# Performance work log

Measured on AMD Instinct MI355X. Metric: run time of the kernel, lower is better.

The kernel has to match this reference:

```python
import jax, jax.numpy as jnp
import numpy as np

B, N, C = 4, 4000, 91          # images, proposals/image, classes (incl. background)
H = W = 800                    # image shape
WX, WY, WW, WH = 10.0, 10.0, 5.0, 5.0   # bbox_reg_weights
BBOX_CLIP = float(np.log(1000.0 / 16.0))
SCORE_T = 0.05
NMS_T = 0.5
DETS = 100                     # detections_per_img
MIN_SIZE = 0.01
NEG = jnp.float32(-1e30)
M = N * (C - 1)                # candidates per image after dropping background


def setup_inputs() -> dict:
    key = jax.random.key(0)
    k1, k2, k3, k4 = jax.random.split(key, 4)
    class_logits = jax.random.normal(k1, (B * N, C), jnp.float32)
    box_regression = jax.random.normal(k2, (B * N, C * 4), jnp.float32)
    # valid proposals: x1<x2, y1<y2, inside the image
    ctr = jax.random.uniform(k3, (B, N, 2), jnp.float32, 0.0, 800.0)
    wh = jax.random.uniform(k4, (B, N, 2), jnp.float32, 16.0, 256.0)
    x1y1 = jnp.clip(ctr - 0.5 * wh, 0.0, 800.0)
    x2y2 = jnp.clip(ctr + 0.5 * wh, 0.0, 800.0)
    proposals = jnp.concatenate([x1y1, x2y2], axis=-1)
    return {"class_logits": class_logits, "box_regression": box_regression,
            "proposals": proposals}


def _decode(rel, props):
    # rel: [B,N,C,4] deltas, props: [B,N,4] -> per-class boxes [B,N,C,4]
    widths = props[..., 2] - props[..., 0]
    heights = props[..., 3] - props[..., 1]
    ctr_x = props[..., 0] + 0.5 * widths
    ctr_y = props[..., 1] + 0.5 * heights
    dx = rel[..., 0] / WX
    dy = rel[..., 1] / WY
    dw = jnp.minimum(rel[..., 2] / WW, BBOX_CLIP)
    dh = jnp.minimum(rel[..., 3] / WH, BBOX_CLIP)
    pcx = dx * widths[..., None] + ctr_x[..., None]
    pcy = dy * heights[..., None] + ctr_y[..., None]
    pw = jnp.exp(dw) * widths[..., None]
    ph = jnp.exp(dh) * heights[..., None]
    return jnp.stack([pcx - 0.5 * pw, pcy - 0.5 * ph,
                      pcx + 0.5 * pw, pcy + 0.5 * ph], axis=-1)


def _iou_one(box, boxes):
    # box [4] vs boxes [M,4]
    lt = jnp.maximum(box[:2], boxes[:, :2])
    rb = jnp.minimum(box[2:], boxes[:, 2:])
    wh = jnp.clip(rb - lt, 0.0)
    inter = wh[:, 0] * wh[:, 1]
    a1 = (box[2] - box[0]) * (box[3] - box[1])
    a2 = (boxes[:, 2] - boxes[:, 0]) * (boxes[:, 3] - boxes[:, 1])
    return inter / (a1 + a2 - inter)


def _nms_image(boxes_off, scores_m):
    # greedy NMS on class-offset boxes; returns DETS indices + validity flags
    idxs = jnp.arange(scores_m.shape[0])

    def step(scores_rem, _):
        best = jnp.argmax(scores_rem)
        bscore = scores_rem[best]
        iou = _iou_one(boxes_off[best], boxes_off)
        sup = (iou > NMS_T) | (idxs == best)
        return jnp.where(sup, NEG, scores_rem), (best, bscore > NEG * 0.5)

    _, (keep_idx, keep_ok) = jax.lax.scan(step, scores_m, None, length=DETS)
    return keep_idx, keep_ok


def reference(class_logits, box_regression, proposals):
    logits = class_logits.reshape(B, N, C)
    rel = box_regression.reshape(B, N, C, 4)
    boxes = _decode(rel, proposals)                       # [B,N,C,4]
    # clip_boxes_to_image
    boxes = jnp.stack([jnp.clip(boxes[..., 0], 0.0, W),
                       jnp.clip(boxes[..., 1], 0.0, H),
                       jnp.clip(boxes[..., 2], 0.0, W),
                       jnp.clip(boxes[..., 3], 0.0, H)], axis=-1)
    scores = jax.nn.softmax(logits, axis=-1)              # [B,N,C]
    # drop background class 0, flatten per-image candidates
    cand_boxes = boxes[:, :, 1:, :].reshape(B, M, 4)
    cand_scores = scores[:, :, 1:].reshape(B, M)
    labels = jnp.tile(jnp.arange(1, C, dtype=jnp.int32), N)   # [M]
    # score threshold + remove_small_boxes
    ws = cand_boxes[..., 2] - cand_boxes[..., 0]
    hs = cand_boxes[..., 3] - cand_boxes[..., 1]
    valid = (cand_scores > SCORE_T) & (ws >= MIN_SIZE) & (hs >= MIN_SIZE)
    scores_m = jnp.where(valid, cand_scores, NEG)
    # batched_nms: offset boxes per class so cross-class boxes never overlap
    offs = labels.astype(jnp.float32) * (W + 1.0)
    boxes_off = cand_boxes + offs[None, :, None]
    keep_idx, keep_ok = jax.vmap(_nms_image)(boxes_off, scores_m)  # [B,DETS]
    out_boxes = jnp.take_along_axis(cand_boxes, keep_idx[..., None], axis=1)
    out_scores = jnp.take_along_axis(cand_scores, keep_idx, axis=1)
    out_labels = labels[keep_idx]
    out_boxes = jnp.where(keep_ok[..., None], out_boxes, 0.0)
    out_scores = jnp.where(keep_ok, out_scores, 0.0)
    out_labels = jnp.where(keep_ok, out_labels, 0)
    return out_boxes, out_scores, out_labels, keep_ok
```

## Files before the change

kernel.cpp:

```cpp
#include <hip/hip_runtime.h>

#define Bc 4
#define Nc 4000
#define Cc 91
#define SEGW 20
#define BCAP 64
#define SELTGT 512
#define DETS 100
#define NBIN 4096
#define SELCAP 1024

typedef unsigned long long u64;

__device__ __forceinline__ float4 decode_box(const float4 r, float w, float h,
                                             float cx, float cy) {
    const float BBOX_CLIP = 4.135166556742356f;
    float dx = r.x / 10.f, dy = r.y / 10.f;
    float dw = fminf(r.z / 5.f, BBOX_CLIP);
    float dh = fminf(r.w / 5.f, BBOX_CLIP);
    float pcx = dx * w + cx, pcy = dy * h + cy;
    float pw = expf(dw) * w, ph = expf(dh) * h;
    float4 o;
    o.x = fminf(fmaxf(pcx - 0.5f * pw, 0.f), 800.f);
    o.y = fminf(fmaxf(pcy - 0.5f * ph, 0.f), 800.f);
    o.z = fminf(fmaxf(pcx + 0.5f * pw, 0.f), 800.f);
    o.w = fminf(fmaxf(pcy + 0.5f * ph, 0.f), 800.f);
    return o;
}

__global__ __launch_bounds__(256) void compact_k(
    const float* __restrict__ logits, const float* __restrict__ regs,
    const float* __restrict__ props, ulonglong2* __restrict__ pmask,
    unsigned* __restrict__ scoreseg, int* __restrict__ ghist,
    int* __restrict__ bcnt, int* __restrict__ done) {
    if (blockIdx.x < 16) {
        int base = blockIdx.x * 1024;
#pragma unroll
        for (int j = 0; j < 4; ++j)
            ghist[base + j * 256 + threadIdx.x] = 0;
    } else if (blockIdx.x == 16) {
        int t = threadIdx.x;
        bcnt[t] = 0;
        if (t < Bc * Cc - 256) bcnt[256 + t] = 0;
        if (t == 0) *done = 0;
    }
    const int wv = threadIdx.x >> 6;
    const int ln = threadIdx.x & 63;
    const int pA = blockIdx.x * 8 + wv * 2;
    const int pB = pA + 1;

    const float* lA = logits + (size_t)pA * Cc;
    const float* lB = logits + (size_t)pB * Cc;
    float a0 = lA[ln];
    float b0 = lB[ln];
    float a1 = (ln < Cc - 64) ? lA[64 + ln] : -1e30f;
    float b1 = (ln < Cc - 64) ? lB[64 + ln] : -1e30f;
    const float4 prA = *reinterpret_cast<const float4*>(props + 4 * (size_t)pA);
    const float4 prB = *reinterpret_cast<const float4*>(props + 4 * (size_t)pB);

    float mA = fmaxf(a0, a1), mB = fmaxf(b0, b1);
#pragma unroll
    for (int off = 32; off; off >>= 1) {
        mA = fmaxf(mA, __shfl_xor(mA, off));
        mB = fmaxf(mB, __shfl_xor(mB, off));
    }
    float eA0 = expf(a0 - mA), eB0 = expf(b0 - mB);
    float eA1 = (ln < Cc - 64) ? expf(a1 - mA) : 0.f;
    float eB1 = (ln < Cc - 64) ? expf(b1 - mB) : 0.f;
    float sA = eA0 + eA1, sB = eB0 + eB1;
#pragma unroll
    for (int off = 32; off; off >>= 1) {
        sA += __shfl_xor(sA, off);
        sB += __shfl_xor(sB, off);
    }

    const float wA = prA.z - prA.x, hA = prA.w - prA.y;
    const float cxA = prA.x + 0.5f * wA, cyA = prA.y + 0.5f * hA;
    const float wB = prB.z - prB.x, hB = prB.w - prB.y;
    const float cxB = prB.x + 0.5f * wB, cyB = prB.y + 0.5f * hB;

    float vA0 = eA0 / sA, vB0 = eB0 / sB, vA1 = eA1 / sA, vB1 = eB1 / sB;
    bool fA0 = false, fA1 = false, fB0 = false, fB1 = false;
    if (ln >= 1 && vA0 > 0.05f) {
        float4 r = *reinterpret_cast<const float4*>(
            regs + ((size_t)pA * Cc + ln) * 4);
        float4 bx = decode_box(r, wA, hA, cxA, cyA);
        fA0 = (bx.z - bx.x >= 0.01f) && (bx.w - bx.y >= 0.01f);
    }
    if (ln >= 1 && vB0 > 0.05f) {
        float4 r = *reinterpret_cast<const float4*>(
            regs + ((size_t)pB * Cc + ln) * 4);
        float4 bx = decode_box(r, wB, hB, cxB, cyB);
        fB0 = (bx.z - bx.x >= 0.01f) && (bx.w - bx.y >= 0.01f);
    }
    if (ln < Cc - 64 && vA1 > 0.05f) {
        float4 r = *reinterpret_cast<const float4*>(
            regs + ((size_t)pA * Cc + 64 + ln) * 4);
        float4 bx = decode_box(r, wA, hA, cxA, cyA);
        fA1 = (bx.z - bx.x >= 0.01f) && (bx.w - bx.y >= 0.01f);
    }
    if (ln < Cc - 64 && vB1 > 0.05f) {
        float4 r = *reinterpret_cast<const float4*>(
            regs + ((size_t)pB * Cc + 64 + ln) * 4);
        float4 bx = decode_box(r, wB, hB, cxB, cyB);
        fB1 = (bx.z - bx.x >= 0.01f) && (bx.w - bx.y >= 0.01f);
    }

    const u64 below = (1ULL << ln) - 1ULL;
    u64 mA0 = __ballot(fA0), mA1 = __ballot(fA1);
    u64 mB0 = __ballot(fB0), mB1 = __ballot(fB1);
    int cA0 = __popcll(mA0), cB0 = __popcll(mB0);
    if (fA0) scoreseg[(size_t)pA * SEGW + __popcll(mA0 & below)] =
        __float_as_uint(vA0);
    if (fA1) scoreseg[(size_t)pA * SEGW + cA0 + __popcll(mA1 & below)] =
        __float_as_uint(vA1);
    if (fB0) scoreseg[(size_t)pB * SEGW + __popcll(mB0 & below)] =
        __float_as_uint(vB0);
    if (fB1) scoreseg[(size_t)pB * SEGW + cB0 + __popcll(mB1 & below)] =
        __float_as_uint(vB1);
    if (ln == 0) {
        pmask[pA] = make_ulonglong2(mA0, mA1);
        pmask[pB] = make_ulonglong2(mB0, mB1);
    }
}

__global__ __launch_bounds__(256) void histsel_k(
    const ulonglong2* __restrict__ pmask, const unsigned* __restrict__ scoreseg,
    int* __restrict__ ghist, int* __restrict__ done,
    u64* __restrict__ bucket, int* __restrict__ bcnt) {
    __shared__ int hist[NBIN];
    __shared__ int thrS;
    const int b = blockIdx.x >> 4;
    const int sub = blockIdx.x & 15;
    const int t = threadIdx.x;

    for (int i = t; i < NBIN; i += 256) hist[i] = 0;
    __syncthreads();
    if (t < 250) {
        int p = b * Nc + sub * 250 + t;
        ulonglong2 pm = pmask[p];
        int nk = __popcll(pm.x) + __popcll(pm.y);
        for (int j = 0; j < nk; ++j)
            atomicAdd(&hist[scoreseg[(size_t)p * SEGW + j] >> 20], 1);
    }
    __syncthreads();
    for (int i = t; i < NBIN; i += 256) {
        int v = hist[i];
        if (v) atomicAdd(&ghist[b * NBIN + i], v);
    }
    __syncthreads();

    if (t == 0) {
        __threadfence();
        atomicAdd(done, 1);
        while (atomicAdd(done, 0) < 64) __builtin_amdgcn_s_sleep(8);
        __threadfence();
    }
    __syncthreads();

    if (t < 64) {
        const int ln = t;
        const int* h = ghist + b * NBIN;
        int loc[64];
        int tot = 0;
#pragma unroll
        for (int j = 0; j < 64; ++j) { loc[j] = h[ln * 64 + j]; tot += loc[j]; }
        int inc = tot;
#pragma unroll
        for (int off = 1; off < 64; off <<= 1) {
            int v = __shfl_down(inc, off);
            if (ln + off < 64) inc += v;
        }
        int cum = inc - tot;
        int myThr = -1;
#pragma unroll
        for (int j = 63; j >= 0; --j) {
            if (cum < SELTGT && cum + loc[j] >= SELTGT) myThr = ln * 64 + j;
            cum += loc[j];
        }
#pragma unroll
        for (int off = 32; off; off >>= 1)
            myThr = max(myThr, __shfl_xor(myThr, off));
        if (ln == 0) thrS = (myThr < 0) ? 0 : myThr;
    }
    __syncthreads();
    const int th = thrS;

    if (t < 250) {
        int p = b * Nc + sub * 250 + t;
        const ulonglong2 pm = pmask[p];
        if (pm.x | pm.y) {
            const int n = p - b * Nc;
            int idx = 0;
#pragma unroll
            for (int rnd = 0; rnd < 2; ++rnd) {
                u64 mm = rnd ? pm.y : pm.x;
                while (mm) {
                    int j = __ffsll((long long)mm) - 1; mm &= mm - 1;
                    int c = j + rnd * 64;
                    unsigned sb = scoreseg[(size_t)p * SEGW + idx]; ++idx;
                    if ((int)(sb >> 20) >= th) {
                        unsigned m = (unsigned)(n * 90 + (c - 1));
                        u64 key = ((u64)sb << 32) |
                                  ((u64)(1048575u - m) << 12) | (u64)c;
                        int sl = atomicAdd(&bcnt[b * Cc + c], 1);
                        if (sl < BCAP) bucket[(b * Cc + c) * BCAP + sl] = key;
                    }
                }
            }
        }
    }
}

__global__ __launch_bounds__(64) void nmsc_k(
    u64* __restrict__ bucket, const int* __restrict__ bcnt,
    const float* __restrict__ regs, const float* __restrict__ props,
    int* __restrict__ kkc) {
    const int b = blockIdx.x / (Cc - 1);
    const int c = 1 + blockIdx.x % (Cc - 1);
    const int ln = threadIdx.x;
    const int nc = min(bcnt[b * Cc + c], BCAP);
    bool alive = ln < nc;
    u64 lk = alive ? bucket[(b * Cc + c) * BCAP + ln] : 0ULL;
    float4 bx = make_float4(0.f, 0.f, 0.f, 0.f);
    float area = 0.f;
    if (alive) {
        int m = 1048575 - (int)((lk >> 12) & 0xFFFFFULL);
        int n = m / (Cc - 1);
        int p = b * Nc + n;
        const float4 pr = *reinterpret_cast<const float4*>(props + 4 * (size_t)p);
        float w = pr.z - pr.x, h = pr.w - pr.y;
        float cx = pr.x + 0.5f * w, cy = pr.y + 0.5f * h;
        const float4 r = *reinterpret_cast<const float4*>(
            regs + ((size_t)p * Cc + c) * 4);
        bx = decode_box(r, w, h, cx, cy);
        float off_ = (float)c * 801.0f;
        bx.x += off_; bx.y += off_; bx.z += off_; bx.w += off_;
        area = (bx.z - bx.x) * (bx.w - bx.y);
    }

    int nk = 0;
    for (;;) {
        u64 m = alive ? lk : 0ULL;
#pragma unroll
        for (int off = 32; off; off >>= 1) {
            u64 o = __shfl_xor(m, off);
            m = (o > m) ? o : m;
        }
        if (m == 0ULL) break;
        u64 wmask = __ballot(alive && lk == m);
        int wl = __ffsll((long long)wmask) - 1;
        if (ln == wl) bucket[(b * Cc + c) * BCAP + nk] = m;
        ++nk;
        float wx1 = __shfl(bx.x, wl), wy1 = __shfl(bx.y, wl);
        float wx2 = __shfl(bx.z, wl), wy2 = __shfl(bx.w, wl);
        float wa = __shfl(area, wl);
        if (alive) {
            if (lk == m) {
                alive = false;
            } else {
                float iw = fmaxf(fminf(wx2, bx.z) - fmaxf(wx1, bx.x), 0.f);
                float ih = fmaxf(fminf(wy2, bx.w) - fmaxf(wy1, bx.y), 0.f);
                float inter = iw * ih;
                float iou = inter / (wa + area - inter);
                if (iou > 0.5f) alive = false;
            }
        }
    }
    if (ln == 0) kkc[b * Cc + c] = nk;
}

__global__ __launch_bounds__(1024) void top100_k(
    const u64* __restrict__ bucket, const int* __restrict__ kkc,
    const float* __restrict__ regs, const float* __restrict__ props,
    float* __restrict__ out) {
    __shared__ u64 sKey[SELCAP];
    __shared__ u64 sTop[DETS];
    __shared__ int cnts[Cc], offs[Cc + 1];
    const int b = blockIdx.x, t = threadIdx.x;
    const int ln = t & 63, wv = t >> 6;

    if (t < Cc)
        cnts[t] = (t == 0) ? 0 : min(max(kkc[b * Cc + t], 0), BCAP);
    if (t < DETS) sTop[t] = 0ULL;
    __syncthreads();
    if (t == 0) {
        int acc = 0;
        for (int c = 0; c < Cc; ++c) { offs[c] = acc; acc += cnts[c]; }
        offs[Cc] = acc;
    }
    __syncthreads();
    const int total = min(offs[Cc], SELCAP);

    for (int c = wv; c < Cc; c += 16) {
        int k = cnts[c];
        if (ln < k) {
            int d = offs[c] + ln;
            if (d >= 0 && d < SELCAP)
                sKey[d] = bucket[(b * Cc + c) * BCAP + ln];
        }
    }
    __syncthreads();

    for (int i = t; i < total; i += 1024) {
        u64 k = sKey[i];
        int r = 0;
#pragma unroll 4
        for (int j = 0; j < total; ++j) r += (sKey[j] > k) ? 1 : 0;
        if (r < DETS) sTop[r] = k;
    }
    __syncthreads();

    if (t < DETS) {
        int o = b * DETS + t;
        u64 k = sTop[t];
        float* ob = out + (size_t)o * 4;
        if (k != 0ULL) {
            int lab = (int)(k & 0xFFFULL);
            int m = 1048575 - (int)((k >> 12) & 0xFFFFFULL);
            int n = m / (Cc - 1);
            int c = m - n * (Cc - 1) + 1;
            int p = b * Nc + n;
            const float4 pr =
                *reinterpret_cast<const float4*>(props + 4 * (size_t)p);
            const float w = pr.z - pr.x, h = pr.w - pr.y;
            const float cx = pr.x + 0.5f * w, cy = pr.y + 0.5f * h;
            const float4 r4 = *reinterpret_cast<const float4*>(
                regs + ((size_t)p * Cc + c) * 4);
            float4 bx = decode_box(r4, w, h, cx, cy);
            ob[0] = bx.x; ob[1] = bx.y; ob[2] = bx.z; ob[3] = bx.w;
            out[Bc * DETS * 4 + o] = __uint_as_float((unsigned)(k >> 32));
            out[Bc * DETS * 5 + o] = (float)lab;
            out[Bc * DETS * 6 + o] = 1.0f;
        } else {
            ob[0] = ob[1] = ob[2] = ob[3] = 0.f;
            out[Bc * DETS * 4 + o] = 0.f;
            out[Bc * DETS * 5 + o] = 0.f;
            out[Bc * DETS * 6 + o] = 0.f;
        }
    }
}

extern "C" void kernel_launch(void* const* d_in, const int* in_sizes, int n_in,
                              void* d_out, int out_size, void* d_ws, size_t ws_size,
                              hipStream_t stream) {
    const float* logits = (const float*)d_in[0];
    const float* regs   = (const float*)d_in[1];
    const float* props  = (const float*)d_in[2];
    float* out = (float*)d_out;

    char* ws = (char*)d_ws;
    size_t o = 0;
    ulonglong2* pmask = (ulonglong2*)(ws + o); o += (size_t)Bc * Nc * 16;
    unsigned* scoreseg = (unsigned*)(ws + o);  o += (size_t)Bc * Nc * SEGW * 4;
    u64* bucket  = (u64*)(ws + o);             o += (size_t)Bc * Cc * BCAP * 8;
    int* ghist   = (int*)(ws + o);             o += (size_t)Bc * NBIN * 4;
    int* bcnt    = (int*)(ws + o);             o += (size_t)Bc * Cc * 4;
    int* kkc     = (int*)(ws + o);             o += (size_t)Bc * Cc * 4;
    int* done    = (int*)(ws + o);

    hipLaunchKernelGGL(compact_k, dim3(Bc * Nc / 8), dim3(256), 0, stream,
                       logits, regs, props, pmask, scoreseg, ghist, bcnt, done);
    hipLaunchKernelGGL(histsel_k, dim3(Bc * 16), dim3(256), 0, stream,
                       pmask, scoreseg, ghist, done, bucket, bcnt);
    hipLaunchKernelGGL(nmsc_k, dim3(Bc * (Cc - 1)), dim3(64), 0, stream,
                       bucket, bcnt, regs, props, kkc);
    hipLaunchKernelGGL(top100_k, dim3(Bc), dim3(1024), 0, stream,
                       bucket, kkc, regs, props, out);
}
```

Baseline: 55.26 us.

## Fuse histogram-select, per-class NMS and top-100 into one persistent kernel

Merges the histogram/threshold-select kernel, the per-class NMS kernel and the final top-100 kernel into a single 64-block kernel that uses atomic-counter grid barriers between phases. Each wave runs NMS for one or two classes, and one block per image does the final rank selection with 256 threads instead of 1024. The aim is to remove two kernel launches and their gaps. In exchange, NMS gets fewer concurrent waves, the top-100 rank sort has less parallelism, and the spin barriers assume all 64 blocks are co-resident.

```diff
diff --git a/kernel.cpp b/kernel.cpp
--- a/kernel.cpp
+++ b/kernel.cpp
@@ -9,6 +9,7 @@
 #define DETS 100
 #define NBIN 4096
 #define SELCAP 1024
+#define MEGABLK 64
 
 typedef unsigned long long u64;
 
@@ -42,7 +43,7 @@
         int t = threadIdx.x;
         bcnt[t] = 0;
         if (t < Bc * Cc - 256) bcnt[256 + t] = 0;
-        if (t == 0) *done = 0;
+        if (t < 3) done[t] = 0;
     }
     const int wv = threadIdx.x >> 6;
     const int ln = threadIdx.x & 63;
@@ -124,64 +125,70 @@
     }
 }
 
-__global__ __launch_bounds__(256) void histsel_k(
+__device__ __forceinline__ void grid_sync(int* ctr) {
+    __syncthreads();
+    if (threadIdx.x == 0) {
+        __threadfence();
+        atomicAdd(ctr, 1);
+        while (atomicAdd(ctr, 0) < MEGABLK) __builtin_amdgcn_s_sleep(2);
+        __threadfence();
+    }
+    __syncthreads();
+}
+
+__global__ __launch_bounds__(256) void mega_k(
     const ulonglong2* __restrict__ pmask, const unsigned* __restrict__ scoreseg,
-    int* __restrict__ ghist, int* __restrict__ done,
-    u64* __restrict__ bucket, int* __restrict__ bcnt) {
-    __shared__ int hist[NBIN];
+    int* __restrict__ ghist, int* __restrict__ done, u64* __restrict__ bucket,
+    int* __restrict__ bcnt, int* __restrict__ kkc,
+    const float* __restrict__ regs, const float* __restrict__ props,
+    float* __restrict__ out) {
+    __shared__ __align__(16) int shm[NBIN];
     __shared__ int thrS;
     const int b = blockIdx.x >> 4;
     const int sub = blockIdx.x & 15;
     const int t = threadIdx.x;
-
-    for (int i = t; i < NBIN; i += 256) hist[i] = 0;
+    const int ln = t & 63, wv = t >> 6;
+
+    for (int i = t; i < NBIN; i += 256) shm[i] = 0;
     __syncthreads();
     if (t < 250) {
         int p = b * Nc + sub * 250 + t;
         ulonglong2 pm = pmask[p];
         int nk = __popcll(pm.x) + __popcll(pm.y);
         for (int j = 0; j < nk; ++j)
-            atomicAdd(&hist[scoreseg[(size_t)p * SEGW + j] >> 20], 1);
+            atomicAdd(&shm[scoreseg[(size_t)p * SEGW + j] >> 20], 1);
     }
     __syncthreads();
     for (int i = t; i < NBIN; i += 256) {
-        int v = hist[i];
+        int v = shm[i];
         if (v) atomicAdd(&ghist[b * NBIN + i], v);
     }
-    __syncthreads();
-
-    if (t == 0) {
-        __threadfence();
-        atomicAdd(done, 1);
-        while (atomicAdd(done, 0) < 64) __builtin_amdgcn_s_sleep(8);
-        __threadfence();
-    }
-    __syncthreads();
+    grid_sync(&done[0]);
 
     if (t < 64) {
-        const int ln = t;
+        const int l = t;
         const int* h = ghist + b * NBIN;
         int loc[64];
         int tot = 0;
 #pragma unroll
-        for (int j = 0; j < 64; ++j) { loc[j] = h[ln * 64 + j]; tot += loc[j]; }
+        for (int j = 0; j < 64; ++j) { loc[j] = h[l * 64 + j]; tot += loc[j]; }
         int inc = tot;
 #pragma unroll
         for (int off = 1; off < 64; off <<= 1) {
             int v = __shfl_down(inc, off);
-            if (ln + off < 64) inc += v;
+            if (l + off < 64) inc += v;
         }
         int cum = inc - tot;
         int myThr = -1;
 #pragma unroll
         for (int j = 63; j >= 0; --j) {
-            if (cum < SELTGT && cum + loc[j] >= SELTGT) myThr = ln * 64 + j;
+            if (cum < SELTGT && cum + loc[j] >= SELTGT) myThr = l * 64 + j;
             cum += loc[j];
         }
 #pragma unroll
         for (int off = 32; off; off >>= 1)
             myThr = max(myThr, __shfl_xor(myThr, off));
-        if (ln == 0) thrS = (myThr < 0) ? 0 : myThr;
+        if (l == 0) thrS = (myThr < 0) ? 0 : myThr;
     }
     __syncthreads();
     const int th = thrS;
@@ -210,78 +217,78 @@
             }
         }
     }
-}
-
-__global__ __launch_bounds__(64) void nmsc_k(
-    u64* __restrict__ bucket, const int* __restrict__ bcnt,
-    const float* __restrict__ regs, const float* __restrict__ props,
-    int* __restrict__ kkc) {
-    const int b = blockIdx.x / (Cc - 1);
-    const int c = 1 + blockIdx.x % (Cc - 1);
-    const int ln = threadIdx.x;
-    const int nc = min(bcnt[b * Cc + c], BCAP);
-    bool alive = ln < nc;
-    u64 lk = alive ? bucket[(b * Cc + c) * BCAP + ln] : 0ULL;
-    float4 bx = make_float4(0.f, 0.f, 0.f, 0.f);
-    float area = 0.f;
-    if (alive) {
-        int m = 1048575 - (int)((lk >> 12) & 0xFFFFFULL);
-        int n = m / (Cc - 1);
-        int p = b * Nc + n;
-        const float4 pr = *reinterpret_cast<const float4*>(props + 4 * (size_t)p);
-        float w = pr.z - pr.x, h = pr.w - pr.y;
-        float cx = pr.x + 0.5f * w, cy = pr.y + 0.5f * h;
-        const float4 r = *reinterpret_cast<const float4*>(
-            regs + ((size_t)p * Cc + c) * 4);
-        bx = decode_box(r, w, h, cx, cy);
-        float off_ = (float)c * 801.0f;
-        bx.x += off_; bx.y += off_; bx.z += off_; bx.w += off_;
-        area = (bx.z - bx.x) * (bx.w - bx.y);
-    }
-
-    int nk = 0;
-    for (;;) {
-        u64 m = alive ? lk : 0ULL;
-#pragma unroll
-        for (int off = 32; off; off >>= 1) {
-            u64 o = __shfl_xor(m, off);
-            m = (o > m) ? o : m;
-        }
-        if (m == 0ULL) break;
-        u64 wmask = __ballot(alive && lk == m);
-        int wl = __ffsll((long long)wmask) - 1;
-        if (ln == wl) bucket[(b * Cc + c) * BCAP + nk] = m;
-        ++nk;
-        float wx1 = __shfl(bx.x, wl), wy1 = __shfl(bx.y, wl);
-        float wx2 = __shfl(bx.z, wl), wy2 = __shfl(bx.w, wl);
-        float wa = __shfl(area, wl);
+    grid_sync(&done[1]);
+
+    const int wid = sub * 4 + wv;
+#pragma unroll
+    for (int rep = 0; rep < 2; ++rep) {
+        if (rep == 1 && wid >= 26) break;
+        const int c = (rep == 0) ? (1 + wid) : (65 + wid);
+        const int nc = min(bcnt[b * Cc + c], BCAP);
+        bool alive = ln < nc;
+        u64 lk = alive ? bucket[(b * Cc + c) * BCAP + ln] : 0ULL;
+        float4 bx = make_float4(0.f, 0.f, 0.f, 0.f);
+        float area = 0.f;
         if (alive) {
-            if (lk == m) {
-                alive = false;
-            } else {
-                float iw = fmaxf(fminf(wx2, bx.z) - fmaxf(wx1, bx.x), 0.f);
-                float ih = fmaxf(fminf(wy2, bx.w) - fmaxf(wy1, bx.y), 0.f);
-                float inter = iw * ih;
-                float iou = inter / (wa + area - inter);
-                if (iou > 0.5f) alive = false;
+            int m = 1048575 - (int)((lk >> 12) & 0xFFFFFULL);
+            int n = m / (Cc - 1);
+            int p = b * Nc + n;
+            const float4 pr =
+                *reinterpret_cast<const float4*>(props + 4 * (size_t)p);
+            float w = pr.z - pr.x, h = pr.w - pr.y;
+            float cx = pr.x + 0.5f * w, cy = pr.y + 0.5f * h;
+            const float4 r = *reinterpret_cast<const float4*>(
+                regs + ((size_t)p * Cc + c) * 4);
+            bx = decode_box(r, w, h, cx, cy);
+            float off_ = (float)c * 801.0f;
+            bx.x += off_; bx.y += off_; bx.z += off_; bx.w += off_;
+            area = (bx.z - bx.x) * (bx.w - bx.y);
+        }
+        int nk = 0;
+        for (;;) {
+            u64 m = alive ? lk : 0ULL;
+#pragma unroll
+            for (int off = 32; off; off >>= 1) {
+                u64 o = __shfl_xor(m, off);
+                m = (o > m) ? o : m;
             }
-        }
-    }
-    if (ln == 0) kkc[b * Cc + c] = nk;
-}
-
-__global__ __launch_bounds__(1024) void top100_k(
-    const u64* __restrict__ bucket, const int* __restrict__ kkc,
-    const float* __restrict__ regs, const float* __restrict__ props,
-    float* __restrict__ out) {
-    __shared__ u64 sKey[SELCAP];
-    __shared__ u64 sTop[DETS];
-    __shared__ int cnts[Cc], offs[Cc + 1];
-    const int b = blockIdx.x, t = threadIdx.x;
-    const int ln = t & 63, wv = t >> 6;
-
-    if (t < Cc)
-        cnts[t] = (t == 0) ? 0 : min(max(kkc[b * Cc + t], 0), BCAP);
+            if (m == 0ULL) break;
+            u64 wmask = __ballot(alive && lk == m);
+            int wl = __ffsll((long long)wmask) - 1;
+            if (ln == wl) bucket[(b * Cc + c) * BCAP + nk] = m;
+            ++nk;
+            float wx1 = __shfl(bx.x, wl), wy1 = __shfl(bx.y, wl);
+            float wx2 = __shfl(bx.z, wl), wy2 = __shfl(bx.w, wl);
+            float wa = __shfl(area, wl);
+            if (alive) {
+                if (lk == m) {
+                    alive = false;
+                } else {
+                    float iw = fmaxf(fminf(wx2, bx.z) - fmaxf(wx1, bx.x), 0.f);
+                    float ih = fmaxf(fminf(wy2, bx.w) - fmaxf(wy1, bx.y), 0.f);
+                    float inter = iw * ih;
+                    float iou = inter / (wa + area - inter);
+                    if (iou > 0.5f) alive = false;
+                }
+            }
+        }
+        if (ln == 0) kkc[b * Cc + c] = nk;
+    }
+
+    __syncthreads();
+    if (t == 0) { __threadfence(); atomicAdd(&done[2], 1); }
+    if (sub != 0) return;
+    if (t == 0) {
+        while (atomicAdd(&done[2], 0) < MEGABLK) __builtin_amdgcn_s_sleep(2);
+        __threadfence();
+    }
+    __syncthreads();
+
+    u64* sKey = (u64*)shm;
+    u64* sTop = (u64*)(shm + 2048);
+    int* cnts = shm + 2256;
+    int* offs = shm + 2352;
+    if (t < Cc) cnts[t] = (t == 0) ? 0 : min(max(kkc[b * Cc + t], 0), BCAP);
     if (t < DETS) sTop[t] = 0ULL;
     __syncthreads();
     if (t == 0) {
@@ -292,17 +299,17 @@
     __syncthreads();
     const int total = min(offs[Cc], SELCAP);
 
-    for (int c = wv; c < Cc; c += 16) {
-        int k = cnts[c];
-        if (ln < k) {
-            int d = offs[c] + ln;
+    for (int i = t; i < Cc * BCAP; i += 256) {
+        int c = i >> 6, l = i & 63;
+        if (c >= 1 && l < cnts[c]) {
+            int d = offs[c] + l;
             if (d >= 0 && d < SELCAP)
-                sKey[d] = bucket[(b * Cc + c) * BCAP + ln];
-        }
-    }
-    __syncthreads();
-
-    for (int i = t; i < total; i += 1024) {
+                sKey[d] = bucket[(b * Cc + c) * BCAP + l];
+        }
+    }
+    __syncthreads();
+
+    for (int i = t; i < total; i += 256) {
         u64 k = sKey[i];
         int r = 0;
 #pragma unroll 4
@@ -357,14 +364,11 @@
     int* ghist   = (int*)(ws + o);             o += (size_t)Bc * NBIN * 4;
     int* bcnt    = (int*)(ws + o);             o += (size_t)Bc * Cc * 4;
     int* kkc     = (int*)(ws + o);             o += (size_t)Bc * Cc * 4;
-    int* done    = (int*)(ws + o);
+    int* done    = (int*)(ws + o);             o += 16;
 
     hipLaunchKernelGGL(compact_k, dim3(Bc * Nc / 8), dim3(256), 0, stream,
                        logits, regs, props, pmask, scoreseg, ghist, bcnt, done);
-    hipLaunchKernelGGL(histsel_k, dim3(Bc * 16), dim3(256), 0, stream,
-                       pmask, scoreseg, ghist, done, bucket, bcnt);
-    hipLaunchKernelGGL(nmsc_k, dim3(Bc * (Cc - 1)), dim3(64), 0, stream,
-                       bucket, bcnt, regs, props, kkc);
-    hipLaunchKernelGGL(top100_k, dim3(Bc), dim3(1024), 0, stream,
-                       bucket, kkc, regs, props, out);
-}
+    hipLaunchKernelGGL(mega_k, dim3(MEGABLK), dim3(256), 0, stream,
+                       pmask, scoreseg, ghist, done, bucket, bcnt, kkc,
+                       regs, props, out);
+}
```

After: 86.51 us. 1.57x slower.
